# Kernel tuning notes

Hardware: AMD Instinct MI355X
Metric: run time of the kernel (lower is better)

The kernel has to match this reference:

```python
import jax, jax.numpy as jnp
import numpy as np

N_NODES = 100000
N_EDGES = 500000
N_GRAPHS = 64
IN_DIM = 512
HID = 256
N_REL = 16


def setup_inputs() -> dict:
    key = jax.random.key(0)
    ks = jax.random.split(key, 14)
    s = 0.02
    inp = {}
    inp["node_feats"] = jax.random.normal(ks[0], (N_NODES, IN_DIM), dtype=jnp.float32)
    inp["edge_index"] = jax.random.randint(ks[1], (2, N_EDGES), 0, N_NODES, dtype=jnp.int64)
    inp["batch_idx"] = jnp.sort(jax.random.randint(ks[2], (N_NODES,), 0, N_GRAPHS, dtype=jnp.int64))
    # GraphConv layer 0: in 512 -> 256; layers 1,2: 256 -> 256
    inp["W_rel0"] = jax.random.normal(ks[3], (IN_DIM, HID), dtype=jnp.float32) * s
    inp["W_root0"] = jax.random.normal(ks[4], (IN_DIM, HID), dtype=jnp.float32) * s
    inp["b0"] = jnp.zeros((HID,), dtype=jnp.float32)
    inp["W_rel1"] = jax.random.normal(ks[5], (HID, HID), dtype=jnp.float32) * s
    inp["W_root1"] = jax.random.normal(ks[6], (HID, HID), dtype=jnp.float32) * s
    inp["b1"] = jnp.zeros((HID,), dtype=jnp.float32)
    inp["W_rel2"] = jax.random.normal(ks[7], (HID, HID), dtype=jnp.float32) * s
    inp["W_root2"] = jax.random.normal(ks[8], (HID, HID), dtype=jnp.float32) * s
    inp["b2"] = jnp.zeros((HID,), dtype=jnp.float32)
    # edge head: concat(src, dst) -> relations
    inp["W_edge"] = jax.random.normal(ks[9], (2 * HID, N_REL), dtype=jnp.float32) * s
    inp["b_edge"] = jnp.zeros((N_REL,), dtype=jnp.float32)
    return inp


def _graph_conv(x, src, dst, W_rel, W_root, b):
    # PyG GraphConv: out_i = W_root x_i + W_rel * sum_{j in N(i)} x_j + b
    agg = jax.ops.segment_sum(x[src], dst, num_segments=x.shape[0])  # [N, d_in]
    return agg @ W_rel + x @ W_root + b


def reference(node_feats, edge_index, batch_idx,
              W_rel0, W_root0, b0, W_rel1, W_root1, b1, W_rel2, W_root2, b2,
              W_edge, b_edge):
    src, dst = edge_index[0], edge_index[1]
    # 3 GraphConv layers with ReLU (dropout is identity at inference)
    x = jax.nn.relu(_graph_conv(node_feats, src, dst, W_rel0, W_root0, b0))
    x = jax.nn.relu(_graph_conv(x, src, dst, W_rel1, W_root1, b1))
    x = jax.nn.relu(_graph_conv(x, src, dst, W_rel2, W_root2, b2))
    # edge head: gather src/dst embeddings, concat, linear
    edge_feats = jnp.concatenate([x[src], x[dst]], axis=1)  # [E, 2*HID]
    edge_logits = edge_feats @ W_edge + b_edge              # [E, N_REL]
    # global mean pool per graph
    sums = jax.ops.segment_sum(x, batch_idx, num_segments=N_GRAPHS)  # [G, HID]
    counts = jax.ops.segment_sum(jnp.ones((x.shape[0], 1), x.dtype), batch_idx, num_segments=N_GRAPHS)
    graph_embed = sums / jnp.maximum(counts, 1.0)
    return edge_logits, graph_embed
```

## Files before the change

### kernel.cpp

```cpp
#include <hip/hip_runtime.h>

#define N_NODES 100000
#define N_EDGES 500000
#define N_GRAPHS 64
#define IN_DIM 512
#define HID 256
#define NREL 16

using short8 = __attribute__((ext_vector_type(8))) short;
using f32x4  = __attribute__((ext_vector_type(4))) float;

__device__ __forceinline__ unsigned short f2bf(float f) {
    union { float f; unsigned u; } v; v.f = f;
    unsigned u = v.u;
    unsigned r = u + 0x7FFF + ((u >> 16) & 1);
    return (unsigned short)(r >> 16);
}
__device__ __forceinline__ float bf2f(unsigned short h) {
    union { unsigned u; float f; } v; v.u = ((unsigned)h) << 16;
    return v.f;
}
__device__ __forceinline__ unsigned cvtpk(float lo, float hi) {
    unsigned r;
    asm("v_cvt_pk_bf16_f32 %0, %1, %2" : "=v"(r) : "v"(lo), "v"(hi));
    return r;
}

__device__ __forceinline__ void gload_lds16(const unsigned short* g, unsigned short* l) {
    __builtin_amdgcn_global_load_lds(
        (const __attribute__((address_space(1))) void*)(g),
        (__attribute__((address_space(3))) void*)(l), 16, 0, 0);
}
__device__ __forceinline__ void gload_lds16f(const float* g, float* l) {
    __builtin_amdgcn_global_load_lds(
        (const __attribute__((address_space(1))) void*)(g),
        (__attribute__((address_space(3))) void*)(l), 16, 0, 0);
}

__global__ void k_makeWt(const float* __restrict__ Wrel, const float* __restrict__ Wroot,
                         unsigned short* __restrict__ Wt, int K) {
    __shared__ float t[64][65];
    int tid = threadIdx.x;
    int tk = blockIdx.x * 64, tn = blockIdx.y * 64;
    const float* Wsrc = (tn < 256) ? Wrel : Wroot;
    int col0 = tn & 255;
    #pragma unroll
    for (int r = 0; r < 16; ++r) {
        int kl = r * 4 + (tid >> 6);
        int nl = tid & 63;
        t[kl][nl] = Wsrc[(size_t)(tk + kl) * 256 + col0 + nl];
    }
    __syncthreads();
    #pragma unroll
    for (int r = 0; r < 16; ++r) {
        int nl = r * 4 + (tid >> 6);
        int kl = tid & 63;
        Wt[(size_t)(tn + nl) * K + tk + kl] = f2bf(t[kl][nl]);
    }
}

__global__ void k_makeWe2T(const float* __restrict__ We, unsigned short* __restrict__ We2T) {
    int idx = blockIdx.x * 256 + threadIdx.x;
    if (idx >= 32 * 256) return;
    int r = idx >> 8, k = idx & 255;
    float v = (r < 16) ? We[k * NREL + r] : We[(256 + k) * NREL + (r - 16)];
    We2T[idx] = f2bf(v);
}

__global__ void k_hist(const int* __restrict__ dstArr, int* __restrict__ counts) {
    int i = blockIdx.x * 256 + threadIdx.x;
    if (i < N_EDGES) atomicAdd(&counts[dstArr[i]], 1);
}

__global__ void k_scanA(const int* __restrict__ counts, int* __restrict__ bsum) {
    __shared__ int ws[4];
    int i = blockIdx.x * 256 + threadIdx.x;
    int v = (i < N_NODES) ? counts[i] : 0;
    for (int o = 32; o; o >>= 1) v += __shfl_down(v, o, 64);
    if ((threadIdx.x & 63) == 0) ws[threadIdx.x >> 6] = v;
    __syncthreads();
    if (threadIdx.x == 0) bsum[blockIdx.x] = ws[0] + ws[1] + ws[2] + ws[3];
}

__global__ void k_scanB(int* __restrict__ bsum, int nb) {
    __shared__ int buf[512];
    int t = threadIdx.x;
    for (int i = t; i < nb; i += 256) buf[i] = bsum[i];
    __syncthreads();
    if (t == 0) { int s = 0; for (int i = 0; i < nb; ++i) { int x = buf[i]; buf[i] = s; s += x; } }
    __syncthreads();
    for (int i = t; i < nb; i += 256) bsum[i] = buf[i];
}

__global__ void k_scanC(const int* __restrict__ counts, const int* __restrict__ bsum,
                        int* __restrict__ offsets, int* __restrict__ cur) {
    __shared__ int ws[4];
    int i = blockIdx.x * 256 + threadIdx.x;
    int lane = threadIdx.x & 63, wid = threadIdx.x >> 6;
    int v = (i < N_NODES) ? counts[i] : 0;
    int x = v;
    for (int o = 1; o < 64; o <<= 1) { int u = __shfl_up(x, o, 64); if (lane >= o) x += u; }
    if (lane == 63) ws[wid] = x;
    __syncthreads();
    if (threadIdx.x == 0) { int s = 0; for (int t = 0; t < 4; ++t) { int tt = ws[t]; ws[t] = s; s += tt; } }
    __syncthreads();
    x += ws[wid];
    x += bsum[blockIdx.x];
    if (i < N_NODES) { offsets[i + 1] = x; cur[i] = x - v; }
    if (i == 0) offsets[0] = 0;
}

__global__ void k_fill(const int* __restrict__ srcArr, const int* __restrict__ dstArr,
                       int* __restrict__ cur, int* __restrict__ csr) {
    int i = blockIdx.x * 256 + threadIdx.x;
    if (i < N_EDGES) {
        int p = atomicAdd(&cur[dstArr[i]], 1);
        csr[p] = srcArr[i];
    }
}

__global__ __launch_bounds__(256) void k_gemm(const unsigned short* __restrict__ A,
                                              const unsigned short* __restrict__ Bt,
                                              unsigned short* __restrict__ Yrel,
                                              unsigned short* __restrict__ Yroot,
                                              int M, int K) {
    __shared__ unsigned short lds[2 * 128 * 64];
    const int tid  = threadIdx.x;
    const int lane = tid & 63;
    const int w    = tid >> 6;
    const int wm   = w >> 1, wn = w & 1;

    int nwg  = gridDim.x;
    int orig = blockIdx.x;
    int q    = nwg >> 3;
    int id   = (orig & 7) * q + (orig >> 3);
    int bm0  = (id >> 2) * 128;
    int bn0  = (id & 3) * 128;

    f32x4 acc[4][4] = {};

    const int nkt = K >> 6;
    for (int kt = 0; kt < nkt; ++kt) {
        int k0 = kt << 6;
        #pragma unroll
        for (int it = 0; it < 4; ++it) {
            int c = (it << 8) + tid;
            int row = c >> 3, kcp = c & 7;
            int kcl = kcp ^ (row & 7);
            int gr = bm0 + row; gr = (gr < M) ? gr : (M - 1);
            gload_lds16(A + (size_t)gr * K + k0 + kcl * 8,
                        &lds[(size_t)((it << 8) + (w << 6)) * 8]);
        }
        #pragma unroll
        for (int it = 0; it < 4; ++it) {
            int c = (it << 8) + tid;
            int row = c >> 3, kcp = c & 7;
            int kcl = kcp ^ (row & 7);
            gload_lds16(Bt + (size_t)(bn0 + row) * K + k0 + kcl * 8,
                        &lds[128 * 64 + (size_t)((it << 8) + (w << 6)) * 8]);
        }
        __syncthreads();
        #pragma unroll
        for (int kk = 0; kk < 2; ++kk) {
            short8 af[4], bfr[4];
            #pragma unroll
            for (int m = 0; m < 4; ++m) {
                int row = wm * 64 + m * 16 + (lane & 15);
                int g = ((kk << 2) + (lane >> 4)) ^ (row & 7);
                af[m] = *(const short8*)&lds[row * 64 + g * 8];
            }
            #pragma unroll
            for (int n = 0; n < 4; ++n) {
                int row = wn * 64 + n * 16 + (lane & 15);
                int g = ((kk << 2) + (lane >> 4)) ^ (row & 7);
                bfr[n] = *(const short8*)&lds[128 * 64 + row * 64 + g * 8];
            }
            #pragma unroll
            for (int m = 0; m < 4; ++m)
                #pragma unroll
                for (int n = 0; n < 4; ++n)
                    acc[m][n] = __builtin_amdgcn_mfma_f32_16x16x32_bf16(af[m], bfr[n], acc[m][n], 0, 0, 0);
        }
        __syncthreads();
    }
    unsigned short* Cout = (bn0 < 256) ? Yrel : Yroot;
    int cb = bn0 & 255;
    #pragma unroll
    for (int m = 0; m < 4; ++m) {
        int row0 = bm0 + wm * 64 + m * 16 + ((lane >> 4) << 2);
        #pragma unroll
        for (int n = 0; n < 4; ++n) {
            int col = cb + wn * 64 + n * 16 + (lane & 15);
            #pragma unroll
            for (int i = 0; i < 4; ++i) {
                int r = row0 + i;
                if (r < M) Cout[(size_t)r * 256 + col] = f2bf(acc[m][n][i]);
            }
        }
    }
}

__global__ __launch_bounds__(256) void k_gemm0(const float* __restrict__ A,
                                               const unsigned short* __restrict__ Bt,
                                               unsigned short* __restrict__ Yrel,
                                               unsigned short* __restrict__ Yroot,
                                               int M) {
    constexpr int K = 512;
    __shared__ float ldsA[128 * 64];
    __shared__ unsigned short ldsB[128 * 64];
    const int tid  = threadIdx.x;
    const int lane = tid & 63;
    const int w    = tid >> 6;
    const int wm   = w >> 1, wn = w & 1;

    int nwg  = gridDim.x;
    int orig = blockIdx.x;
    int q    = nwg >> 3;
    int id   = (orig & 7) * q + (orig >> 3);
    int bm0  = (id >> 2) * 128;
    int bn0  = (id & 3) * 128;

    f32x4 acc[4][4] = {};

    const int nkt = K >> 6;
    for (int kt = 0; kt < nkt; ++kt) {
        int k0 = kt << 6;
        #pragma unroll
        for (int it = 0; it < 8; ++it) {
            int gi = (it << 8) + tid;
            int row = gi >> 4, gp = gi & 15;
            int gs = gp ^ (row & 15);
            int gr = bm0 + row; gr = (gr < M) ? gr : (M - 1);
            gload_lds16f(A + (size_t)gr * K + k0 + gs * 4,
                         &ldsA[(size_t)((it << 8) + (w << 6)) * 4]);
        }
        #pragma unroll
        for (int it = 0; it < 4; ++it) {
            int c = (it << 8) + tid;
            int row = c >> 3, kcp = c & 7;
            int kcl = kcp ^ (row & 7);
            gload_lds16(Bt + (size_t)(bn0 + row) * K + k0 + kcl * 8,
                        &ldsB[(size_t)((it << 8) + (w << 6)) * 8]);
        }
        __syncthreads();
        #pragma unroll
        for (int kk = 0; kk < 2; ++kk) {
            short8 af[4], bfr[4];
            #pragma unroll
            for (int m = 0; m < 4; ++m) {
                int row = wm * 64 + m * 16 + (lane & 15);
                int c = (kk << 2) + (lane >> 4);
                int g0 = (2 * c) ^ (row & 15);
                int g1 = (2 * c + 1) ^ (row & 15);
                f32x4 fa = *(const f32x4*)&ldsA[row * 64 + g0 * 4];
                f32x4 fb = *(const f32x4*)&ldsA[row * 64 + g1 * 4];
                union { short8 s8; unsigned u[4]; } vv;
                vv.u[0] = cvtpk(fa[0], fa[1]);
                vv.u[1] = cvtpk(fa[2], fa[3]);
                vv.u[2] = cvtpk(fb[0], fb[1]);
                vv.u[3] = cvtpk(fb[2], fb[3]);
                af[m] = vv.s8;
            }
            #pragma unroll
            for (int n = 0; n < 4; ++n) {
                int row = wn * 64 + n * 16 + (lane & 15);
                int g = ((kk << 2) + (lane >> 4)) ^ (row & 7);
                bfr[n] = *(const short8*)&ldsB[row * 64 + g * 8];
            }
            #pragma unroll
            for (int m = 0; m < 4; ++m)
                #pragma unroll
                for (int n = 0; n < 4; ++n)
                    acc[m][n] = __builtin_amdgcn_mfma_f32_16x16x32_bf16(af[m], bfr[n], acc[m][n], 0, 0, 0);
        }
        __syncthreads();
    }
    unsigned short* Cout = (bn0 < 256) ? Yrel : Yroot;
    int cb = bn0 & 255;
    #pragma unroll
    for (int m = 0; m < 4; ++m) {
        int row0 = bm0 + wm * 64 + m * 16 + ((lane >> 4) << 2);
        #pragma unroll
        for (int n = 0; n < 4; ++n) {
            int col = cb + wn * 64 + n * 16 + (lane & 15);
            #pragma unroll
            for (int i = 0; i < 4; ++i) {
                int r = row0 + i;
                if (r < M) Cout[(size_t)r * 256 + col] = f2bf(acc[m][n][i]);
            }
        }
    }
}

__device__ __forceinline__ void acc4(float4& a, ushort4 v) {
    a.x += bf2f(v.x); a.y += bf2f(v.y); a.z += bf2f(v.z); a.w += bf2f(v.w);
}

__global__ void k_combine(const unsigned short* __restrict__ yrel,
                          const unsigned short* __restrict__ yroot,
                          const int* __restrict__ offs,
                          const int* __restrict__ csr, const float* __restrict__ bias,
                          unsigned short* __restrict__ xout) {
    int node = blockIdx.x * 4 + (threadIdx.x >> 6);
    if (node >= N_NODES) return;
    int lane = threadIdx.x & 63;
    int d = lane * 4;
    int j0 = offs[node], j1 = offs[node + 1];
    float4 a0 = {0,0,0,0}, a1 = {0,0,0,0}, a2 = {0,0,0,0}, a3 = {0,0,0,0};
    int j = j0;
    for (; j + 4 <= j1; j += 4) {
        int s0 = csr[j], s1 = csr[j + 1], s2 = csr[j + 2], s3 = csr[j + 3];
        ushort4 v0 = *(const ushort4*)(yrel + (size_t)s0 * 256 + d);
        ushort4 v1 = *(const ushort4*)(yrel + (size_t)s1 * 256 + d);
        ushort4 v2 = *(const ushort4*)(yrel + (size_t)s2 * 256 + d);
        ushort4 v3 = *(const ushort4*)(yrel + (size_t)s3 * 256 + d);
        acc4(a0, v0); acc4(a1, v1); acc4(a2, v2); acc4(a3, v3);
    }
    for (; j < j1; ++j) {
        int s = csr[j];
        acc4(a0, *(const ushort4*)(yrel + (size_t)s * 256 + d));
    }
    a0.x += a1.x + a2.x + a3.x;
    a0.y += a1.y + a2.y + a3.y;
    a0.z += a1.z + a2.z + a3.z;
    a0.w += a1.w + a2.w + a3.w;
    ushort4 rr = *(const ushort4*)(yroot + (size_t)node * 256 + d);
    float4 bb = *(const float4*)(bias + d);
    ushort4 pk;
    pk.x = f2bf(fmaxf(a0.x + bf2f(rr.x) + bb.x, 0.f));
    pk.y = f2bf(fmaxf(a0.y + bf2f(rr.y) + bb.y, 0.f));
    pk.z = f2bf(fmaxf(a0.z + bf2f(rr.z) + bb.z, 0.f));
    pk.w = f2bf(fmaxf(a0.w + bf2f(rr.w) + bb.w, 0.f));
    *(ushort4*)(xout + (size_t)node * HID + d) = pk;
}

__global__ void k_proj(const unsigned short* __restrict__ x,
                       const unsigned short* __restrict__ We2T,
                       float* __restrict__ P) {
    int lane = threadIdx.x & 63;
    int g = blockIdx.x * 4 + (threadIdx.x >> 6);
    if (g * 16 >= N_NODES) return;
    int n0 = g * 16;
    short8 bfr[2][8];
    #pragma unroll
    for (int cg = 0; cg < 2; ++cg)
        #pragma unroll
        for (int ks = 0; ks < 8; ++ks)
            bfr[cg][ks] = *(const short8*)&We2T[(size_t)(cg * 16 + (lane & 15)) * 256 + ks * 32 + ((lane >> 4) << 3)];
    f32x4 acc[2] = {};
    const size_t rb = (size_t)(n0 + (lane & 15)) * 256 + ((lane >> 4) << 3);
    #pragma unroll
    for (int ks = 0; ks < 8; ++ks) {
        short8 af = *(const short8*)&x[rb + ks * 32];
        acc[0] = __builtin_amdgcn_mfma_f32_16x16x32_bf16(af, bfr[0][ks], acc[0], 0, 0, 0);
        acc[1] = __builtin_amdgcn_mfma_f32_16x16x32_bf16(af, bfr[1][ks], acc[1], 0, 0, 0);
    }
    #pragma unroll
    for (int cg = 0; cg < 2; ++cg) {
        #pragma unroll
        for (int i = 0; i < 4; ++i) {
            int n = n0 + ((lane >> 4) << 2) + i;
            P[(size_t)n * 32 + cg * 16 + (lane & 15)] = acc[cg][i];
        }
    }
}

__global__ void k_edge_add(const float* __restrict__ P,
                           const int* __restrict__ srcArr, const int* __restrict__ dstArr,
                           const float* __restrict__ b_edge, float* __restrict__ out) {
    int e = blockIdx.x * 256 + threadIdx.x;
    if (e >= N_EDGES) return;
    int s = srcArr[e], d = dstArr[e];
    const float4* ps = (const float4*)(P + (size_t)s * 32);
    const float4* pd = (const float4*)(P + (size_t)d * 32 + 16);
    const float4* bb = (const float4*)b_edge;
    float4* po = (float4*)(out + (size_t)e * 16);
    #pragma unroll
    for (int i = 0; i < 4; ++i) {
        float4 a = ps[i], b = pd[i], c = bb[i];
        float4 rr;
        rr.x = a.x + b.x + c.x; rr.y = a.y + b.y + c.y;
        rr.z = a.z + b.z + c.z; rr.w = a.w + b.w + c.w;
        po[i] = rr;
    }
}

__global__ void k_pool_sum(const unsigned short* __restrict__ x, const int* __restrict__ batch,
                           float* __restrict__ sums) {
    const int CH = 32;
    int w = threadIdx.x >> 6, lane = threadIdx.x & 63;
    int n0 = blockIdx.x * (4 * CH) + w * CH;
    if (n0 >= N_NODES) return;
    int n1 = n0 + CH; if (n1 > N_NODES) n1 = N_NODES;
    int d = lane * 4;
    float a0 = 0.f, a1 = 0.f, a2 = 0.f, a3 = 0.f;
    int gcur = batch[n0];
    for (int n = n0; n < n1; ++n) {
        int g = batch[n];
        if (g != gcur) {
            float* p = &sums[gcur * HID + d];
            atomicAdd(p + 0, a0); atomicAdd(p + 1, a1);
            atomicAdd(p + 2, a2); atomicAdd(p + 3, a3);
            a0 = a1 = a2 = a3 = 0.f; gcur = g;
        }
        ushort4 v = *(const ushort4*)&x[(size_t)n * HID + d];
        a0 += bf2f(v.x); a1 += bf2f(v.y); a2 += bf2f(v.z); a3 += bf2f(v.w);
    }
    float* p = &sums[gcur * HID + d];
    atomicAdd(p + 0, a0); atomicAdd(p + 1, a1);
    atomicAdd(p + 2, a2); atomicAdd(p + 3, a3);
}

__device__ __forceinline__ int lowerBound(const int* a, int n, int key) {
    int lo = 0, hi = n;
    while (lo < hi) { int mid = (lo + hi) >> 1; if (a[mid] < key) lo = mid + 1; else hi = mid; }
    return lo;
}

__global__ void k_pool_final(const float* __restrict__ sums, const int* __restrict__ batch,
                             float* __restrict__ out) {
    int g = blockIdx.x, d = threadIdx.x;
    int lo = lowerBound(batch, N_NODES, g);
    int hi = lowerBound(batch, N_NODES, g + 1);
    float cnt = (float)(hi - lo);
    out[(size_t)g * HID + d] = sums[g * HID + d] / fmaxf(cnt, 1.0f);
}

extern "C" void kernel_launch(void* const* d_in, const int* in_sizes, int n_in,
                              void* d_out, int out_size, void* d_ws, size_t ws_size,
                              hipStream_t stream) {
    const float* node_feats = (const float*)d_in[0];
    const int*   edge_index = (const int*)d_in[1];
    const int*   batch_idx  = (const int*)d_in[2];
    const float* W_rel0  = (const float*)d_in[3];
    const float* W_root0 = (const float*)d_in[4];
    const float* b0      = (const float*)d_in[5];
    const float* W_rel1  = (const float*)d_in[6];
    const float* W_root1 = (const float*)d_in[7];
    const float* b1      = (const float*)d_in[8];
    const float* W_rel2  = (const float*)d_in[9];
    const float* W_root2 = (const float*)d_in[10];
    const float* b2      = (const float*)d_in[11];
    const float* W_edge  = (const float*)d_in[12];
    const float* b_edge  = (const float*)d_in[13];

    const int* src = edge_index;
    const int* dst = edge_index + N_EDGES;

    char* ws = (char*)d_ws;
    size_t off = 0;
    auto alloc = [&](size_t bytes) -> char* {
        off = (off + 255) & ~(size_t)255;
        char* p = ws + off;
        off += bytes;
        return p;
    };
    unsigned short* xA    = (unsigned short*)alloc((size_t)N_NODES * HID * 2);
    unsigned short* xB    = (unsigned short*)alloc((size_t)N_NODES * HID * 2);
    unsigned short* Yrel  = (unsigned short*)alloc((size_t)N_NODES * HID * 2);
    unsigned short* Yroot = (unsigned short*)alloc((size_t)N_NODES * HID * 2);
    unsigned short* Wt0   = (unsigned short*)alloc(512 * 512 * 2);
    unsigned short* Wt1   = (unsigned short*)alloc(512 * 256 * 2);
    unsigned short* Wt2   = (unsigned short*)alloc(512 * 256 * 2);
    unsigned short* We2T  = (unsigned short*)alloc(32 * 256 * 2);
    float* P     = (float*)alloc((size_t)N_NODES * 32 * 4);
    int* counts  = (int*)alloc((size_t)N_NODES * 4);
    int* offsets = (int*)alloc((size_t)(N_NODES + 1) * 4);
    int* cur     = (int*)alloc((size_t)N_NODES * 4);
    int* csr     = (int*)alloc((size_t)N_EDGES * 4);
    int* bsum    = (int*)alloc(512 * 4);
    float* sums  = (float*)alloc(N_GRAPHS * HID * 4);

    const int nscan = (N_NODES + 255) / 256;

    hipMemsetAsync(counts, 0, (size_t)N_NODES * 4, stream);
    hipMemsetAsync(sums, 0, N_GRAPHS * HID * 4, stream);

    k_makeWt<<<dim3(8, 8), 256, 0, stream>>>(W_rel0, W_root0, Wt0, 512);
    k_makeWt<<<dim3(4, 8), 256, 0, stream>>>(W_rel1, W_root1, Wt1, 256);
    k_makeWt<<<dim3(4, 8), 256, 0, stream>>>(W_rel2, W_root2, Wt2, 256);
    k_makeWe2T<<<32, 256, 0, stream>>>(W_edge, We2T);

    k_hist<<<(N_EDGES + 255) / 256, 256, 0, stream>>>(dst, counts);
    k_scanA<<<nscan, 256, 0, stream>>>(counts, bsum);
    k_scanB<<<1, 256, 0, stream>>>(bsum, nscan);
    k_scanC<<<nscan, 256, 0, stream>>>(counts, bsum, offsets, cur);
    k_fill<<<(N_EDGES + 255) / 256, 256, 0, stream>>>(src, dst, cur, csr);

    const int gemmGrid = ((N_NODES + 127) / 128) * 4;
    k_gemm0<<<gemmGrid, 256, 0, stream>>>(node_feats, Wt0, Yrel, Yroot, N_NODES);
    k_combine<<<(N_NODES + 3) / 4, 256, 0, stream>>>(Yrel, Yroot, offsets, csr, b0, xB);
    k_gemm<<<gemmGrid, 256, 0, stream>>>(xB, Wt1, Yrel, Yroot, N_NODES, 256);
    k_combine<<<(N_NODES + 3) / 4, 256, 0, stream>>>(Yrel, Yroot, offsets, csr, b1, xA);
    k_gemm<<<gemmGrid, 256, 0, stream>>>(xA, Wt2, Yrel, Yroot, N_NODES, 256);
    k_combine<<<(N_NODES + 3) / 4, 256, 0, stream>>>(Yrel, Yroot, offsets, csr, b2, xB);

    float* out_logits = (float*)d_out;
    k_proj<<<(N_NODES / 16 + 3) / 4, 256, 0, stream>>>(xB, We2T, P);
    k_edge_add<<<(N_EDGES + 255) / 256, 256, 0, stream>>>(P, src, dst, b_edge, out_logits);

    float* out_embed = (float*)d_out + (size_t)N_EDGES * NREL;
    k_pool_sum<<<(N_NODES + 127) / 128, 256, 0, stream>>>(xB, batch_idx, sums);
    k_pool_final<<<N_GRAPHS, 256, 0, stream>>>(sums, batch_idx, out_embed);
}
```

Measured before the change: 513.1 us.

## Keep full weight half resident in registers for layer 1-2 GEMMs

Replaces the 128x128 tiled GEMM for the 256-dim layers with a kernel that loads a full 256x256 weight half into LDS once, keeps each wave's B fragments in registers, and streams 16-row A tiles through a double-buffered LDS slot. Each block covers 256 rows and one output half (rel or root). This removes repeated weight tile reloads and the per-k-step barrier structure, but it uses about 144 KB of LDS per block, which limits occupancy to one block per CU. It also needs a barrier per 16-row step and writes output with scattered 2-byte stores.

```diff
diff --git a/kernel.cpp b/kernel.cpp
--- a/kernel.cpp
+++ b/kernel.cpp
@@ -119,84 +119,78 @@
     }
 }
 
-__global__ __launch_bounds__(256) void k_gemm(const unsigned short* __restrict__ A,
-                                              const unsigned short* __restrict__ Bt,
-                                              unsigned short* __restrict__ Yrel,
-                                              unsigned short* __restrict__ Yroot,
-                                              int M, int K) {
-    __shared__ unsigned short lds[2 * 128 * 64];
+__global__ __launch_bounds__(512) void k_gemm_br(const unsigned short* __restrict__ A,
+                                                 const unsigned short* __restrict__ Bt,
+                                                 unsigned short* __restrict__ Yrel,
+                                                 unsigned short* __restrict__ Yroot,
+                                                 int M) {
+    constexpr int K = 256;
+    __shared__ unsigned short Bl[256 * 256];
+    __shared__ unsigned short Al[2][16 * 256];
     const int tid  = threadIdx.x;
     const int lane = tid & 63;
     const int w    = tid >> 6;
-    const int wm   = w >> 1, wn = w & 1;
-
-    int nwg  = gridDim.x;
-    int orig = blockIdx.x;
-    int q    = nwg >> 3;
-    int id   = (orig & 7) * q + (orig >> 3);
-    int bm0  = (id >> 2) * 128;
-    int bn0  = (id & 3) * 128;
-
-    f32x4 acc[4][4] = {};
-
-    const int nkt = K >> 6;
-    for (int kt = 0; kt < nkt; ++kt) {
-        int k0 = kt << 6;
-        #pragma unroll
-        for (int it = 0; it < 4; ++it) {
-            int c = (it << 8) + tid;
-            int row = c >> 3, kcp = c & 7;
-            int kcl = kcp ^ (row & 7);
-            int gr = bm0 + row; gr = (gr < M) ? gr : (M - 1);
-            gload_lds16(A + (size_t)gr * K + k0 + kcl * 8,
-                        &lds[(size_t)((it << 8) + (w << 6)) * 8]);
-        }
-        #pragma unroll
-        for (int it = 0; it < 4; ++it) {
-            int c = (it << 8) + tid;
-            int row = c >> 3, kcp = c & 7;
-            int kcl = kcp ^ (row & 7);
-            gload_lds16(Bt + (size_t)(bn0 + row) * K + k0 + kcl * 8,
-                        &lds[128 * 64 + (size_t)((it << 8) + (w << 6)) * 8]);
-        }
-        __syncthreads();
-        #pragma unroll
-        for (int kk = 0; kk < 2; ++kk) {
-            short8 af[4], bfr[4];
-            #pragma unroll
-            for (int m = 0; m < 4; ++m) {
-                int row = wm * 64 + m * 16 + (lane & 15);
-                int g = ((kk << 2) + (lane >> 4)) ^ (row & 7);
-                af[m] = *(const short8*)&lds[row * 64 + g * 8];
+    const int h    = blockIdx.x & 1;
+    const int bm0  = (blockIdx.x >> 1) * 256;
+    unsigned short* Cout = h ? Yroot : Yrel;
+
+    #pragma unroll
+    for (int i = 0; i < 16; ++i) {
+        int gi = (i << 9) + tid;
+        int row = gi >> 5, gp = gi & 31;
+        gload_lds16(Bt + (size_t)(h * 256 + row) * K + gp * 8,
+                    &Bl[(size_t)((i << 9) + (w << 6)) * 8]);
+    }
+    {
+        int row = tid >> 5, gp = tid & 31;
+        int gs = gp ^ (row & 7);
+        int gr = bm0 + row; if (gr >= M) gr = M - 1;
+        gload_lds16(A + (size_t)gr * K + gs * 8, &Al[0][(size_t)(w << 6) * 8]);
+    }
+    __syncthreads();
+
+    short8 bf[2][8];
+    #pragma unroll
+    for (int n = 0; n < 2; ++n)
+        #pragma unroll
+        for (int kc = 0; kc < 8; ++kc) {
+            int brow = (w << 5) + (n << 4) + (lane & 15);
+            bf[n][kc] = *(const short8*)&Bl[brow * 256 + (kc << 5) + ((lane >> 4) << 3)];
+        }
+
+    int cur = 0;
+    #pragma unroll 1
+    for (int p = 0; p < 16; ++p) {
+        if (p + 1 < 16) {
+            int row = tid >> 5, gp = tid & 31;
+            int gs = gp ^ (row & 7);
+            int gr = bm0 + (p + 1) * 16 + row; if (gr >= M) gr = M - 1;
+            gload_lds16(A + (size_t)gr * K + gs * 8, &Al[cur ^ 1][(size_t)(w << 6) * 8]);
+        }
+        f32x4 a0 = {}, a1 = {};
+        const unsigned short* Ap = Al[cur];
+        #pragma unroll
+        for (int kc = 0; kc < 8; ++kc) {
+            int row = lane & 15;
+            int pos = ((kc << 2) + (lane >> 4)) ^ (row & 7);
+            short8 af = *(const short8*)&Ap[row * 256 + pos * 8];
+            a0 = __builtin_amdgcn_mfma_f32_16x16x32_bf16(af, bf[0][kc], a0, 0, 0, 0);
+            a1 = __builtin_amdgcn_mfma_f32_16x16x32_bf16(af, bf[1][kc], a1, 0, 0, 0);
+        }
+        int r0 = bm0 + p * 16 + ((lane >> 4) << 2);
+        int c0 = (w << 5) + (lane & 15);
+        #pragma unroll
+        for (int i = 0; i < 4; ++i) {
+            int r = r0 + i;
+            if (r < M) {
+                Cout[(size_t)r * 256 + c0]      = f2bf(a0[i]);
+                Cout[(size_t)r * 256 + c0 + 16] = f2bf(a1[i]);
             }
-            #pragma unroll
-            for (int n = 0; n < 4; ++n) {
-                int row = wn * 64 + n * 16 + (lane & 15);
-                int g = ((kk << 2) + (lane >> 4)) ^ (row & 7);
-                bfr[n] = *(const short8*)&lds[128 * 64 + row * 64 + g * 8];
-            }
-            #pragma unroll
-            for (int m = 0; m < 4; ++m)
-                #pragma unroll
-                for (int n = 0; n < 4; ++n)
-                    acc[m][n] = __builtin_amdgcn_mfma_f32_16x16x32_bf16(af[m], bfr[n], acc[m][n], 0, 0, 0);
-        }
-        __syncthreads();
-    }
-    unsigned short* Cout = (bn0 < 256) ? Yrel : Yroot;
-    int cb = bn0 & 255;
-    #pragma unroll
-    for (int m = 0; m < 4; ++m) {
-        int row0 = bm0 + wm * 64 + m * 16 + ((lane >> 4) << 2);
-        #pragma unroll
-        for (int n = 0; n < 4; ++n) {
-            int col = cb + wn * 64 + n * 16 + (lane & 15);
-            #pragma unroll
-            for (int i = 0; i < 4; ++i) {
-                int r = row0 + i;
-                if (r < M) Cout[(size_t)r * 256 + col] = f2bf(acc[m][n][i]);
-            }
-        }
+        }
+        asm volatile("s_waitcnt vmcnt(0) lgkmcnt(0)" ::: "memory");
+        __builtin_amdgcn_s_barrier();
+        __builtin_amdgcn_sched_barrier(0);
+        cur ^= 1;
     }
 }
 
@@ -488,11 +482,12 @@
     k_fill<<<(N_EDGES + 255) / 256, 256, 0, stream>>>(src, dst, cur, csr);
 
     const int gemmGrid = ((N_NODES + 127) / 128) * 4;
+    const int brGrid   = ((N_NODES + 255) / 256) * 2;
     k_gemm0<<<gemmGrid, 256, 0, stream>>>(node_feats, Wt0, Yrel, Yroot, N_NODES);
     k_combine<<<(N_NODES + 3) / 4, 256, 0, stream>>>(Yrel, Yroot, offsets, csr, b0, xB);
-    k_gemm<<<gemmGrid, 256, 0, stream>>>(xB, Wt1, Yrel, Yroot, N_NODES, 256);
+    k_gemm_br<<<brGrid, 512, 0, stream>>>(xB, Wt1, Yrel, Yroot, N_NODES);
     k_combine<<<(N_NODES + 3) / 4, 256, 0, stream>>>(Yrel, Yroot, offsets, csr, b1, xA);
-    k_gemm<<<gemmGrid, 256, 0, stream>>>(xA, Wt2, Yrel, Yroot, N_NODES, 256);
+    k_gemm_br<<<brGrid, 512, 0, stream>>>(xA, Wt2, Yrel, Yroot, N_NODES);
     k_combine<<<(N_NODES + 3) / 4, 256, 0, stream>>>(Yrel, Yroot, offsets, csr, b2, xB);
 
     float* out_logits = (float*)d_out;
```

New measurement: 569.9 us. 11.1% more time.
